# Performance work log

Measured on AMD Instinct MI355X. Metric: run time of the kernel, lower is better.

## Reference

```python
import jax, jax.numpy as jnp
import numpy as np

N_TOKEN = 4096
INPUT_DIM = 1024
QUERY_DIM = 1024
VALUE_DIM = 1024


def setup_inputs() -> dict:
    key = jax.random.key(0)
    ks = jax.random.split(key, 7)
    s = 0.02
    return {
        "x": jax.random.normal(ks[0], (N_TOKEN, INPUT_DIM), dtype=jnp.float32),
        "W_q": jax.random.normal(ks[1], (INPUT_DIM, QUERY_DIM), dtype=jnp.float32) * s,
        "b_q": jax.random.normal(ks[2], (QUERY_DIM,), dtype=jnp.float32) * s,
        "W_k": jax.random.normal(ks[3], (INPUT_DIM, QUERY_DIM), dtype=jnp.float32) * s,
        "b_k": jax.random.normal(ks[4], (QUERY_DIM,), dtype=jnp.float32) * s,
        "W_v": jax.random.normal(ks[5], (INPUT_DIM, VALUE_DIM), dtype=jnp.float32) * s,
        "b_v": jax.random.normal(ks[6], (VALUE_DIM,), dtype=jnp.float32) * s,
    }


def reference(x, W_q, b_q, W_k, b_k, W_v, b_v):
    # Projections: [n, d_in] @ [d_in, d_q/v]
    Q = x @ W_q + b_q
    K = x @ W_k + b_k
    V = x @ W_v + b_v
    n, q_dim = Q.shape
    scale = 1.0 / jnp.sqrt(jnp.asarray(q_dim, dtype=Q.dtype))
    scores = (Q @ K.T) * scale  # [n, n]
    # causal mask: positions j > i get -inf
    causal = jnp.tril(jnp.ones((n, n), dtype=bool))
    scores = jnp.where(causal, scores, -jnp.inf)
    attn = jax.nn.softmax(scores, axis=-1)
    return attn @ V
```

## Files before the change

### kernel.cpp

```cpp
#include <hip/hip_runtime.h>

#define N_TOK 4096
#define DIM   1024

typedef __bf16 bf16x8 __attribute__((ext_vector_type(8)));
typedef float  f32x4  __attribute__((ext_vector_type(4)));

__device__ __forceinline__ unsigned short f2bf(float f) {
  union { float f; unsigned u; } v; v.f = f;
  unsigned u = v.u;
  return (unsigned short)((u + 0x7fffu + ((u >> 16) & 1u)) >> 16);
}
__device__ __forceinline__ float bf2f(unsigned short h) {
  union { unsigned u; float f; } v; v.u = ((unsigned)h) << 16;
  return v.f;
}

__device__ __forceinline__ void gll16(const unsigned short* g,
                                      unsigned short* l) {
  __builtin_amdgcn_global_load_lds(
      (const __attribute__((address_space(1))) unsigned int*)g,
      (__attribute__((address_space(3))) unsigned int*)l, 16, 0, 0);
}

#define PB_CVT 0
#define PB_TQ 2048
#define PB_ZERO 5120
#define PB_LSUM 5888
#define PB_BIAS 5892
#define PB_TOTAL 5895

__global__ void prep(const float* __restrict__ x, const float* __restrict__ Wq,
                     const float* __restrict__ Wk, const float* __restrict__ Wv,
                     const float* __restrict__ bq, const float* __restrict__ bk,
                     const float* __restrict__ bv,
                     unsigned short* __restrict__ xb,
                     unsigned short* __restrict__ Wt,
                     float* __restrict__ out, float* __restrict__ ball,
                     float* __restrict__ Lsum) {
  const int b = blockIdx.x;
  const int t = threadIdx.x;
  if (b < PB_TQ) {
    const int i = ((b - PB_CVT) * 256 + t) * 8;
    float4 v0 = *(const float4*)(x + i);
    float4 v1 = *(const float4*)(x + i + 4);
    ushort4 r0, r1;
    r0.x = f2bf(v0.x); r0.y = f2bf(v0.y); r0.z = f2bf(v0.z); r0.w = f2bf(v0.w);
    r1.x = f2bf(v1.x); r1.y = f2bf(v1.y); r1.z = f2bf(v1.z); r1.w = f2bf(v1.w);
    *(ushort4*)(xb + i) = r0;
    *(ushort4*)(xb + i + 4) = r1;
  } else if (b < PB_ZERO) {
    const int which = (b - PB_TQ) >> 10;
    const int lb = (b - PB_TQ) & 1023;
    const float* W = (which == 0) ? Wq : (which == 1) ? Wk : Wv;
    unsigned short* D = Wt + (size_t)which * 1024 * 1024;
    __shared__ float tile[32][33];
    const int bx = (lb & 31) * 32, by = (lb >> 5) * 32;
    const int tx = t & 31, ty = t >> 5;
    for (int r = ty; r < 32; r += 8)
      tile[r][tx] = W[(size_t)(by + r) * DIM + bx + tx];
    __syncthreads();
    for (int r = ty; r < 32; r += 8)
      D[(size_t)(bx + r) * DIM + by + tx] = f2bf(tile[tx][r]);
  } else if (b < PB_LSUM) {
    float4* p = (float4*)(out + (size_t)1024 * DIM);
    const int i = ((b - PB_ZERO) * 256 + t) * 4;
#pragma unroll
    for (int c = 0; c < 4; c++) p[i + c] = make_float4(0.f, 0.f, 0.f, 0.f);
  } else if (b < PB_BIAS) {
    const int i = ((b - PB_LSUM) * 256 + t) * 4;
    *(float4*)(Lsum + i) = make_float4(0.f, 0.f, 0.f, 0.f);
  } else {
    const int i = ((b - PB_BIAS) * 256 + t) * 4;
#pragma unroll
    for (int c = 0; c < 4; c++) {
      const int k = i + c;
      if (k < 3072)
        ball[k] = (k < 1024) ? bq[k] * 0.03125f
                             : ((k < 2048) ? bk[k - 1024] : bv[k - 2048]);
    }
  }
}

__global__ void transpose_bf16(const unsigned short* __restrict__ V, int ldv,
                               unsigned short* __restrict__ Vt, int ldvt) {
  __shared__ unsigned short tile[32][33];
  int bx = blockIdx.x * 32;
  int by = blockIdx.y * 32;
  int tx = threadIdx.x, ty = threadIdx.y;
  for (int r = ty; r < 32; r += 8)
    tile[r][tx] = V[(size_t)(by + r) * ldv + bx + tx];
  __syncthreads();
  for (int r = ty; r < 32; r += 8)
    Vt[(size_t)(bx + r) * ldvt + by + tx] = tile[tx][r];
}

#define BK 64

template <int EPI>
__global__ void gemm_tn(const unsigned short* __restrict__ A,
                        const unsigned short* __restrict__ B,
                        void* __restrict__ Cout,
                        const float* __restrict__ bias,
                        float* __restrict__ Lsum,
                        int K, int lda, int ldb, int ldc) {
  int bm, bn, kbeg, kend;
  bool single = true;
  if (EPI == 3) {
    bn = blockIdx.x; bm = blockIdx.y;
    const int Keff = (bm + 1) * 128;
    kbeg = blockIdx.z * 1024;
    if (kbeg >= Keff) return;
    kend = min(kbeg + 1024, Keff);
    single = (Keff <= 1024);
  } else {
    bm = blockIdx.y; bn = blockIdx.x;
    if (EPI == 2 && bn > bm) return;
    kbeg = 0; kend = K;
  }

  __shared__ __align__(16) unsigned short smA[128 * 64];
  __shared__ __align__(16) unsigned short smB[128 * 64];

  const int t = threadIdx.x;
  const int lane = t & 63, w = t >> 6;
  const int wm = (w & 1) * 64, wn = (w >> 1) * 64;

  f32x4 acc[4][4] = {};

  const unsigned short* Ab = A + (size_t)bm * 128 * lda;
  const unsigned short* Bb = B + (size_t)bn * 128 * ldb;

  const int rA = wm + (lane & 15);
  const int rB = wn + (lane & 15);
  const int kquad = (lane >> 4) << 3;

  const int lr = lane >> 3;
  const int g8 = (lane & 7) << 3;
  const unsigned short* pa = Ab + (size_t)lr * lda + g8 + kbeg;
  const unsigned short* pb = Bb + (size_t)lr * ldb + g8 + kbeg;

  for (int k0 = kbeg; k0 < kend; k0 += BK) {
    __syncthreads();
#pragma unroll
    for (int m = 0; m < 4; m++) {
      const int r0 = (w << 5) + (m << 3);
      gll16(pa + (size_t)r0 * lda, smA + r0 * 64);
      gll16(pb + (size_t)r0 * ldb, smB + r0 * 64);
    }
    pa += BK; pb += BK;
    __syncthreads();

#pragma unroll
    for (int kk = 0; kk < BK; kk += 32) {
      bf16x8 af[4], bfr[4];
      const int kof = kk + kquad;
#pragma unroll
      for (int i = 0; i < 4; i++)
        af[i] = *(const bf16x8*)(&smA[(rA + i * 16) * 64 + kof]);
#pragma unroll
      for (int j = 0; j < 4; j++)
        bfr[j] = *(const bf16x8*)(&smB[(rB + j * 16) * 64 + kof]);
#pragma unroll
      for (int i = 0; i < 4; i++)
#pragma unroll
        for (int j = 0; j < 4; j++)
          acc[i][j] = __builtin_amdgcn_mfma_f32_16x16x32_bf16(af[i], bfr[j],
                                                              acc[i][j], 0, 0, 0);
    }
  }

  float* Cf = (float*)Cout;
  unsigned short* Ch = (unsigned short*)Cout;
  const int colbase = bn * 128 + wn + (lane & 15);
  const int rowbase = bm * 128 + wm + ((lane >> 4) << 2);

  if (EPI == 0) {
#pragma unroll
    for (int i = 0; i < 4; i++)
#pragma unroll
      for (int j = 0; j < 4; j++) {
        const int gc = colbase + j * 16;
        const float cs = (gc < 1024) ? 0.03125f : 1.0f;
#pragma unroll
        for (int r = 0; r < 4; r++) {
          const int gr = rowbase + i * 16 + r;
          Ch[(size_t)gr * ldc + gc] = f2bf(acc[i][j][r] * cs + bias[gc]);
        }
      }
  } else if (EPI == 2) {
    __syncthreads();
    float* Lp = (float*)smA;
    if (t < 128) Lp[t] = 0.f;
    __syncthreads();
#pragma unroll
    for (int i = 0; i < 4; i++)
#pragma unroll
      for (int r = 0; r < 4; r++) {
        const int gr = rowbase + i * 16 + r;
        float sj = 0.f;
#pragma unroll
        for (int j = 0; j < 4; j++) {
          const int gc = colbase + j * 16;
          unsigned short h = 0;
          if (gc <= gr) h = f2bf(__expf(acc[i][j][r]));
          Ch[(size_t)gr * ldc + gc] = h;
          sj += bf2f(h);
        }
        sj += __shfl_xor(sj, 1);
        sj += __shfl_xor(sj, 2);
        sj += __shfl_xor(sj, 4);
        sj += __shfl_xor(sj, 8);
        if ((lane & 15) == 0)
          atomicAdd(&Lp[wm + ((lane >> 4) << 2) + i * 16 + r], sj);
      }
    __syncthreads();
    if (t < 128) atomicAdd(&Lsum[bm * 128 + t], Lp[t]);
  } else {
#pragma unroll
    for (int i = 0; i < 4; i++)
#pragma unroll
      for (int r = 0; r < 4; r++) {
        const int gr = rowbase + i * 16 + r;
        const float linv = 1.0f / Lsum[gr];
#pragma unroll
        for (int j = 0; j < 4; j++) {
          const int gc = colbase + j * 16;
          const float v = acc[i][j][r] * linv;
          if (single)
            Cf[(size_t)gr * ldc + gc] = v;
          else
            atomicAdd(&Cf[(size_t)gr * ldc + gc], v);
        }
      }
  }
}

extern "C" void kernel_launch(void* const* d_in, const int* in_sizes, int n_in,
                              void* d_out, int out_size, void* d_ws,
                              size_t ws_size, hipStream_t stream) {
  (void)in_sizes; (void)n_in; (void)out_size; (void)ws_size;
  const float* x  = (const float*)d_in[0];
  const float* Wq = (const float*)d_in[1];
  const float* bq = (const float*)d_in[2];
  const float* Wk = (const float*)d_in[3];
  const float* bk = (const float*)d_in[4];
  const float* Wv = (const float*)d_in[5];
  const float* bv = (const float*)d_in[6];
  float* out = (float*)d_out;

  const size_t M1 = (size_t)1024 * 1024;
  unsigned short* xb   = (unsigned short*)d_ws;
  unsigned short* Wt   = xb + 4 * M1;
  unsigned short* Call = Wt + 3 * M1;
  unsigned short* Sb   = Call + 12 * M1;
  float* ball          = (float*)(Sb + 16 * M1);
  float* Lsum          = ball + 3072;

  prep<<<PB_TOTAL, 256, 0, stream>>>(x, Wq, Wk, Wv, bq, bk, bv, xb, Wt, out,
                                     ball, Lsum);
  gemm_tn<0><<<dim3(24, 32), 256, 0, stream>>>(xb, Wt, Call, ball, nullptr,
                                               DIM, DIM, DIM, 3 * DIM);
  transpose_bf16<<<dim3(32, 128), dim3(32, 8), 0, stream>>>(Call + 2048,
                                                            3 * DIM, xb, N_TOK);
  gemm_tn<2><<<dim3(32, 32), 256, 0, stream>>>(Call, Call + 1024, Sb, nullptr,
                                               Lsum, DIM, 3 * DIM, 3 * DIM,
                                               N_TOK);
  gemm_tn<3><<<dim3(8, 32, 4), 256, 0, stream>>>(Sb, xb, out, nullptr, Lsum,
                                                 N_TOK, N_TOK, N_TOK, DIM);
}
```

Baseline: 221.7 us.

## Double-buffer GEMM LDS tiles with async prefetch and XOR swizzle

The GEMM main loop now uses two LDS buffers per operand and issues the global-to-LDS loads for the next K tile before computing on the current one. Manual vmcnt waits and barriers replace the two __syncthreads per iteration. An XOR swizzle on the column offset is applied on both the load and the read side to reduce LDS bank conflicts. LDS use doubles, which may lower occupancy, and the waitcnt-based synchronisation depends on an exact count of outstanding loads.

```diff
diff --git a/kernel.cpp b/kernel.cpp
--- a/kernel.cpp
+++ b/kernel.cpp
@@ -96,6 +96,7 @@
 }
 
 #define BK 64
+#define TSZ (128 * 64)
 
 template <int EPI>
 __global__ void gemm_tn(const unsigned short* __restrict__ A,
@@ -119,8 +120,8 @@
     kbeg = 0; kend = K;
   }
 
-  __shared__ __align__(16) unsigned short smA[128 * 64];
-  __shared__ __align__(16) unsigned short smB[128 * 64];
+  __shared__ __align__(16) unsigned short smA[2 * TSZ];
+  __shared__ __align__(16) unsigned short smB[2 * TSZ];
 
   const int t = threadIdx.x;
   const int lane = t & 63, w = t >> 6;
@@ -134,33 +135,52 @@
   const int rA = wm + (lane & 15);
   const int rB = wn + (lane & 15);
   const int kquad = (lane >> 4) << 3;
+  const int swz = (lane & 7) << 3;
 
   const int lr = lane >> 3;
-  const int g8 = (lane & 7) << 3;
+  const int g8 = (((lane & 7) ^ lr) << 3);
   const unsigned short* pa = Ab + (size_t)lr * lda + g8 + kbeg;
   const unsigned short* pb = Bb + (size_t)lr * ldb + g8 + kbeg;
 
-  for (int k0 = kbeg; k0 < kend; k0 += BK) {
-    __syncthreads();
+  const int nt = (kend - kbeg) / BK;
+
+  auto stage = [&](int c, int tt) {
+    const unsigned short* qa = pa + (size_t)tt * BK;
+    const unsigned short* qb = pb + (size_t)tt * BK;
+    unsigned short* da = smA + c * TSZ;
+    unsigned short* db = smB + c * TSZ;
 #pragma unroll
     for (int m = 0; m < 4; m++) {
       const int r0 = (w << 5) + (m << 3);
-      gll16(pa + (size_t)r0 * lda, smA + r0 * 64);
-      gll16(pb + (size_t)r0 * ldb, smB + r0 * 64);
-    }
-    pa += BK; pb += BK;
-    __syncthreads();
-
+      gll16(qa + (size_t)r0 * lda, da + r0 * 64);
+      gll16(qb + (size_t)r0 * ldb, db + r0 * 64);
+    }
+  };
+
+  stage(0, 0);
+  int cur = 0;
+  for (int it = 0; it < nt; ++it) {
+    if (it + 1 < nt) {
+      stage(cur ^ 1, it + 1);
+      asm volatile("s_waitcnt vmcnt(8)" ::: "memory");
+    } else {
+      asm volatile("s_waitcnt vmcnt(0)" ::: "memory");
+    }
+    __builtin_amdgcn_s_barrier();
+    __builtin_amdgcn_sched_barrier(0);
+
+    const unsigned short* sa = smA + cur * TSZ;
+    const unsigned short* sb = smB + cur * TSZ;
 #pragma unroll
     for (int kk = 0; kk < BK; kk += 32) {
       bf16x8 af[4], bfr[4];
-      const int kof = kk + kquad;
+      const int kof = (kk + kquad) ^ swz;
 #pragma unroll
       for (int i = 0; i < 4; i++)
-        af[i] = *(const bf16x8*)(&smA[(rA + i * 16) * 64 + kof]);
+        af[i] = *(const bf16x8*)(&sa[(rA + i * 16) * 64 + kof]);
 #pragma unroll
       for (int j = 0; j < 4; j++)
-        bfr[j] = *(const bf16x8*)(&smB[(rB + j * 16) * 64 + kof]);
+        bfr[j] = *(const bf16x8*)(&sb[(rB + j * 16) * 64 + kof]);
 #pragma unroll
       for (int i = 0; i < 4; i++)
 #pragma unroll
@@ -168,6 +188,8 @@
           acc[i][j] = __builtin_amdgcn_mfma_f32_16x16x32_bf16(af[i], bfr[j],
                                                               acc[i][j], 0, 0, 0);
     }
+    asm volatile("s_waitcnt lgkmcnt(0)\ns_barrier" ::: "memory");
+    cur ^= 1;
   }
 
   float* Cf = (float*)Cout;
```

New measurement: 238.5 us. 7.6% more time.

## Use 256x256 double-buffered GEMM tiles with XCD remap and LDS swizzle

Applied to the files above, without the earlier changes.

The shared GEMM kernel moves from 128x128 tiles with 4 waves to 256x256 tiles with 8 waves. LDS is double-buffered so the next K-tile is prefetched while MFMAs run, with s_setprio around the compute phases. An XOR swizzle is added to LDS addressing to reduce bank conflicts, and workgroup IDs are remapped so neighbouring tiles land on the same XCD for better L2 reuse. The trade-offs are fewer workgroups (less parallelism for the causal/triangular grids), much more LDS per block, and higher register pressure from 8x4 accumulators.

```diff
diff --git a/kernel.cpp b/kernel.cpp
--- a/kernel.cpp
+++ b/kernel.cpp
@@ -98,103 +98,175 @@
 #define BK 64
 
 template <int EPI>
-__global__ void gemm_tn(const unsigned short* __restrict__ A,
-                        const unsigned short* __restrict__ B,
-                        void* __restrict__ Cout,
-                        const float* __restrict__ bias,
-                        float* __restrict__ Lsum,
-                        int K, int lda, int ldb, int ldc) {
-  int bm, bn, kbeg, kend;
+__global__ __launch_bounds__(512, 2) void gemm_tn(
+    const unsigned short* __restrict__ A, const unsigned short* __restrict__ B,
+    void* __restrict__ Cout, const float* __restrict__ bias,
+    float* __restrict__ Lsum, int K, int lda, int ldb, int ldc) {
+  const int nwg = gridDim.x * gridDim.y;
+  const int orig = blockIdx.y * gridDim.x + blockIdx.x;
+  const int q8 = nwg >> 3, r8 = nwg & 7;
+  const int xcd = orig & 7;
+  const int wg = ((xcd < r8) ? xcd * (q8 + 1) : r8 * (q8 + 1) + (xcd - r8) * q8)
+                 + (orig >> 3);
+  int bm = wg / gridDim.x;
+  int bn = wg % gridDim.x;
+
+  int kbeg, kend;
   bool single = true;
   if (EPI == 3) {
-    bn = blockIdx.x; bm = blockIdx.y;
-    const int Keff = (bm + 1) * 128;
+    const int Keff = (bm + 1) * 256;
     kbeg = blockIdx.z * 1024;
     if (kbeg >= Keff) return;
     kend = min(kbeg + 1024, Keff);
     single = (Keff <= 1024);
   } else {
-    bm = blockIdx.y; bn = blockIdx.x;
     if (EPI == 2 && bn > bm) return;
     kbeg = 0; kend = K;
   }
 
-  __shared__ __align__(16) unsigned short smA[128 * 64];
-  __shared__ __align__(16) unsigned short smB[128 * 64];
+  __shared__ __align__(16) unsigned short smA[2][256 * 64];
+  __shared__ __align__(16) unsigned short smB[2][256 * 64];
 
   const int t = threadIdx.x;
   const int lane = t & 63, w = t >> 6;
-  const int wm = (w & 1) * 64, wn = (w >> 1) * 64;
-
-  f32x4 acc[4][4] = {};
-
-  const unsigned short* Ab = A + (size_t)bm * 128 * lda;
-  const unsigned short* Bb = B + (size_t)bn * 128 * ldb;
-
-  const int rA = wm + (lane & 15);
-  const int rB = wn + (lane & 15);
-  const int kquad = (lane >> 4) << 3;
+  const int wr = w >> 2;
+  const int wc = w & 3;
+  const int lane15 = lane & 15;
+  const int kq = (lane >> 4) << 3;
+  const int swz = (lane & 7) << 3;
+
+  f32x4 acc[8][4] = {};
 
   const int lr = lane >> 3;
-  const int g8 = (lane & 7) << 3;
-  const unsigned short* pa = Ab + (size_t)lr * lda + g8 + kbeg;
-  const unsigned short* pb = Bb + (size_t)lr * ldb + g8 + kbeg;
-
-  for (int k0 = kbeg; k0 < kend; k0 += BK) {
-    __syncthreads();
-#pragma unroll
-    for (int m = 0; m < 4; m++) {
-      const int r0 = (w << 5) + (m << 3);
-      gll16(pa + (size_t)r0 * lda, smA + r0 * 64);
-      gll16(pb + (size_t)r0 * ldb, smB + r0 * 64);
+  const int g8 = ((lane & 7) ^ lr) << 3;
+  const unsigned short* srcA =
+      A + (size_t)((size_t)bm * 256 + (w << 4) + lr) * lda + g8 + kbeg;
+  const unsigned short* srcB =
+      B + (size_t)((size_t)bn * 256 + (w << 4) + lr) * ldb + g8 + kbeg;
+
+  const int nt = (kend - kbeg) / BK;
+
+  auto stg = [&](int bufi, int tt, int half) {
+#pragma unroll
+    for (int c = 0; c < 2; c++) {
+      const int rb = half * 128 + (w << 4) + (c << 3);
+      const size_t go = (size_t)(half * 128 + (c << 3));
+      gll16(srcA + go * lda + (size_t)tt * BK, &smA[bufi][rb * 64]);
+      gll16(srcB + go * ldb + (size_t)tt * BK, &smB[bufi][rb * 64]);
     }
-    pa += BK; pb += BK;
-    __syncthreads();
-
-#pragma unroll
-    for (int kk = 0; kk < BK; kk += 32) {
-      bf16x8 af[4], bfr[4];
-      const int kof = kk + kquad;
-#pragma unroll
-      for (int i = 0; i < 4; i++)
-        af[i] = *(const bf16x8*)(&smA[(rA + i * 16) * 64 + kof]);
+  };
+
+  stg(0, 0, 0);
+  stg(0, 0, 1);
+  asm volatile("s_waitcnt vmcnt(0)" ::: "memory");
+  __builtin_amdgcn_s_barrier();
+
+  int buf = 0;
+  for (int tt = 0; tt < nt; ++tt) {
+    const int nx = tt + 1;
+    const unsigned short* sA = smA[buf];
+    const unsigned short* sB = smB[buf];
+    bf16x8 bA[4], bB0[4], bB1[4];
+    const int kof0 = kq ^ swz;
+    const int kof1 = (32 + kq) ^ swz;
+
+#pragma unroll
+    for (int i = 0; i < 4; i++)
+      bA[i] = *(const bf16x8*)&sA[(wr * 128 + i * 16 + lane15) * 64 + kof0];
+#pragma unroll
+    for (int j = 0; j < 4; j++)
+      bB0[j] = *(const bf16x8*)&sB[(wc * 64 + j * 16 + lane15) * 64 + kof0];
+    if (nx < nt) stg(buf ^ 1, nx, 0);
+    __builtin_amdgcn_s_barrier();
+    asm volatile("s_waitcnt lgkmcnt(0)" ::: "memory");
+    __builtin_amdgcn_s_setprio(1);
+#pragma unroll
+    for (int i = 0; i < 4; i++)
 #pragma unroll
       for (int j = 0; j < 4; j++)
-        bfr[j] = *(const bf16x8*)(&smB[(rB + j * 16) * 64 + kof]);
-#pragma unroll
-      for (int i = 0; i < 4; i++)
-#pragma unroll
-        for (int j = 0; j < 4; j++)
-          acc[i][j] = __builtin_amdgcn_mfma_f32_16x16x32_bf16(af[i], bfr[j],
-                                                              acc[i][j], 0, 0, 0);
-    }
+        acc[i][j] = __builtin_amdgcn_mfma_f32_16x16x32_bf16(bA[i], bB0[j],
+                                                            acc[i][j], 0, 0, 0);
+    __builtin_amdgcn_s_setprio(0);
+    __builtin_amdgcn_s_barrier();
+
+#pragma unroll
+    for (int i = 0; i < 4; i++)
+      bA[i] = *(const bf16x8*)&sA[(wr * 128 + i * 16 + lane15) * 64 + kof1];
+#pragma unroll
+    for (int j = 0; j < 4; j++)
+      bB1[j] = *(const bf16x8*)&sB[(wc * 64 + j * 16 + lane15) * 64 + kof1];
+    if (nx < nt) stg(buf ^ 1, nx, 1);
+    __builtin_amdgcn_s_barrier();
+    asm volatile("s_waitcnt lgkmcnt(0)" ::: "memory");
+    __builtin_amdgcn_s_setprio(1);
+#pragma unroll
+    for (int i = 0; i < 4; i++)
+#pragma unroll
+      for (int j = 0; j < 4; j++)
+        acc[i][j] = __builtin_amdgcn_mfma_f32_16x16x32_bf16(bA[i], bB1[j],
+                                                            acc[i][j], 0, 0, 0);
+    __builtin_amdgcn_s_setprio(0);
+    __builtin_amdgcn_s_barrier();
+
+#pragma unroll
+    for (int i = 0; i < 4; i++)
+      bA[i] = *(const bf16x8*)&sA[(wr * 128 + 64 + i * 16 + lane15) * 64 + kof0];
+    __builtin_amdgcn_s_barrier();
+    asm volatile("s_waitcnt lgkmcnt(0)" ::: "memory");
+    __builtin_amdgcn_s_setprio(1);
+#pragma unroll
+    for (int i = 0; i < 4; i++)
+#pragma unroll
+      for (int j = 0; j < 4; j++)
+        acc[4 + i][j] = __builtin_amdgcn_mfma_f32_16x16x32_bf16(
+            bA[i], bB0[j], acc[4 + i][j], 0, 0, 0);
+    __builtin_amdgcn_s_setprio(0);
+    __builtin_amdgcn_s_barrier();
+
+#pragma unroll
+    for (int i = 0; i < 4; i++)
+      bA[i] = *(const bf16x8*)&sA[(wr * 128 + 64 + i * 16 + lane15) * 64 + kof1];
+    __builtin_amdgcn_s_barrier();
+    asm volatile("s_waitcnt lgkmcnt(0)" ::: "memory");
+    __builtin_amdgcn_s_setprio(1);
+#pragma unroll
+    for (int i = 0; i < 4; i++)
+#pragma unroll
+      for (int j = 0; j < 4; j++)
+        acc[4 + i][j] = __builtin_amdgcn_mfma_f32_16x16x32_bf16(
+            bA[i], bB1[j], acc[4 + i][j], 0, 0, 0);
+    __builtin_amdgcn_s_setprio(0);
+    if (nx < nt) asm volatile("s_waitcnt vmcnt(0)" ::: "memory");
+    __builtin_amdgcn_s_barrier();
+    buf ^= 1;
   }
 
   float* Cf = (float*)Cout;
   unsigned short* Ch = (unsigned short*)Cout;
-  const int colbase = bn * 128 + wn + (lane & 15);
-  const int rowbase = bm * 128 + wm + ((lane >> 4) << 2);
+  const int colbase = bn * 256 + wc * 64 + lane15;
+  const int rowbase = bm * 256 + wr * 128 + ((lane >> 4) << 2);
 
   if (EPI == 0) {
 #pragma unroll
-    for (int i = 0; i < 4; i++)
+    for (int i = 0; i < 8; i++)
 #pragma unroll
       for (int j = 0; j < 4; j++) {
         const int gc = colbase + j * 16;
         const float cs = (gc < 1024) ? 0.03125f : 1.0f;
+        const float bs = bias[gc];
 #pragma unroll
         for (int r = 0; r < 4; r++) {
           const int gr = rowbase + i * 16 + r;
-          Ch[(size_t)gr * ldc + gc] = f2bf(acc[i][j][r] * cs + bias[gc]);
+          Ch[(size_t)gr * ldc + gc] = f2bf(acc[i][j][r] * cs + bs);
         }
       }
   } else if (EPI == 2) {
     __syncthreads();
     float* Lp = (float*)smA;
-    if (t < 128) Lp[t] = 0.f;
+    if (t < 256) Lp[t] = 0.f;
     __syncthreads();
 #pragma unroll
-    for (int i = 0; i < 4; i++)
+    for (int i = 0; i < 8; i++)
 #pragma unroll
       for (int r = 0; r < 4; r++) {
         const int gr = rowbase + i * 16 + r;
@@ -211,14 +283,14 @@
         sj += __shfl_xor(sj, 2);
         sj += __shfl_xor(sj, 4);
         sj += __shfl_xor(sj, 8);
-        if ((lane & 15) == 0)
-          atomicAdd(&Lp[wm + ((lane >> 4) << 2) + i * 16 + r], sj);
+        if (lane15 == 0)
+          atomicAdd(&Lp[wr * 128 + i * 16 + ((lane >> 4) << 2) + r], sj);
       }
     __syncthreads();
-    if (t < 128) atomicAdd(&Lsum[bm * 128 + t], Lp[t]);
+    if (t < 256) atomicAdd(&Lsum[bm * 256 + t], Lp[t]);
   } else {
 #pragma unroll
-    for (int i = 0; i < 4; i++)
+    for (int i = 0; i < 8; i++)
 #pragma unroll
       for (int r = 0; r < 4; r++) {
         const int gr = rowbase + i * 16 + r;
@@ -259,13 +331,13 @@
 
   prep<<<PB_TOTAL, 256, 0, stream>>>(x, Wq, Wk, Wv, bq, bk, bv, xb, Wt, out,
                                      ball, Lsum);
-  gemm_tn<0><<<dim3(24, 32), 256, 0, stream>>>(xb, Wt, Call, ball, nullptr,
+  gemm_tn<0><<<dim3(12, 16), 512, 0, stream>>>(xb, Wt, Call, ball, nullptr,
                                                DIM, DIM, DIM, 3 * DIM);
   transpose_bf16<<<dim3(32, 128), dim3(32, 8), 0, stream>>>(Call + 2048,
                                                             3 * DIM, xb, N_TOK);
-  gemm_tn<2><<<dim3(32, 32), 256, 0, stream>>>(Call, Call + 1024, Sb, nullptr,
+  gemm_tn<2><<<dim3(16, 16), 512, 0, stream>>>(Call, Call + 1024, Sb, nullptr,
                                                Lsum, DIM, 3 * DIM, 3 * DIM,
                                                N_TOK);
-  gemm_tn<3><<<dim3(8, 32, 4), 256, 0, stream>>>(Sb, xb, out, nullptr, Lsum,
+  gemm_tn<3><<<dim3(4, 16, 4), 512, 0, stream>>>(Sb, xb, out, nullptr, Lsum,
                                                  N_TOK, N_TOK, N_TOK, DIM);
 }
```

Result: slower. 227.3 us (+2.5%).
